# Performance work log

Hardware: AMD Instinct MI355X
Metric: run time of the kernel (lower is better)

Reference implementation:

```python
import jax, jax.numpy as jnp
import numpy as np

N = 100000   # nodes
E = 1600000  # edges (avg degree 16)
G = 64       # graphs in the batch


def setup_inputs() -> dict:
    key = jax.random.key(0)
    ks = jax.random.split(key, 12)
    x = jax.random.normal(ks[0], (N, 1), jnp.float32)
    src = jax.random.randint(ks[1], (E,), 0, N)
    dst = jax.random.randint(ks[2], (E,), 0, N)
    batch = jnp.sort(jax.random.randint(ks[3], (N,), 0, G))
    def glorot(k, shape):
        fan_in, fan_out = shape
        lim = (6.0 / (fan_in + fan_out)) ** 0.5
        return jax.random.uniform(k, shape, jnp.float32, -lim, lim)
    return {
        "x": x, "src": src, "dst": dst, "batch": batch,
        "W1": glorot(ks[4], (1, 100)),   "b1": jnp.zeros((100,), jnp.float32),
        "W2": glorot(ks[5], (100, 200)), "b2": jnp.zeros((200,), jnp.float32),
        "Wl1": glorot(ks[6], (200, 100)), "bl1": jnp.zeros((100,), jnp.float32),
        "Wl2": glorot(ks[7], (100, 1)),   "bl2": jnp.zeros((1,), jnp.float32),
    }


def gcn_layer(x, W, b, src, dst, n_nodes):
    """PyG GCNConv: linear, then sym-normalized aggregation with self-loops, then bias."""
    h = x @ W                                   # [N, out]
    deg = jax.ops.segment_sum(jnp.ones_like(src, dtype=h.dtype), dst,
                              num_segments=n_nodes) + 1.0  # +1 for self-loop
    dinv = jax.lax.rsqrt(deg)                   # [N]
    norm = dinv[src] * dinv[dst]                # [E]
    agg = jax.ops.segment_sum(h[src] * norm[:, None], dst, num_segments=n_nodes)
    agg = agg + h * (dinv * dinv)[:, None]      # self-loop message
    return agg + b


def reference(x, src, dst, batch, W1, b1, W2, b2, Wl1, bl1, Wl2, bl2):
    n = x.shape[0]
    h = jax.nn.silu(gcn_layer(x, W1, b1, src, dst, n))       # [N,100]
    h = jax.nn.silu(gcn_layer(h, W2, b2, src, dst, n))       # [N,200]
    counts = jax.ops.segment_sum(jnp.ones((n,), h.dtype), batch, num_segments=G)
    pooled = jax.ops.segment_sum(h, batch, num_segments=G) / jnp.maximum(counts, 1.0)[:, None]
    h = jax.nn.silu(pooled @ Wl1 + bl1)                      # [G,100]
    out = h @ Wl2 + bl2                                      # [G,1]
    return out.squeeze(-1)                                   # [G]
```

## Files before the change

kernel.cpp:

```cpp
#include <hip/hip_runtime.h>
#include <math.h>

#define F1 100
#define F2 200
#define KM 12
#define BW_LOG 9
#define BW 512

__device__ __forceinline__ float siluf(float v) {
    return v / (1.0f + expf(-v));
}
__device__ __forceinline__ float silu_fast(float v) {
    return __fdividef(v, 1.0f + __expf(-v));
}

#define PREP_BLOCKS 16
__global__ __launch_bounds__(256) void k_prep(
    const int* __restrict__ batch, int N, int G, int nbk,
    int* __restrict__ starts, int* __restrict__ counts,
    double* __restrict__ pooled, int* __restrict__ bcnt, unsigned* __restrict__ amax) {
    int t = threadIdx.x;
    int b = blockIdx.x;
    for (int idx = b * 256 + t; idx < G * F2; idx += PREP_BLOCKS * 256)
        pooled[idx] = 0.0;
    if (b == 1) {
        for (int i = t; i < nbk; i += 256) bcnt[i] = 0;
        if (t == 0) *amax = 0u;
    }
    if (b == 0) {
        if (t <= G) {
            int lo = 0, hi = N;
            while (lo < hi) {
                int mid = (lo + hi) >> 1;
                if (batch[mid] < t) lo = mid + 1; else hi = mid;
            }
            starts[t] = lo;
        }
        __syncthreads();
        if (t < G) counts[t] = starts[t + 1] - starts[t];
    }
}

__global__ __launch_bounds__(256) void k_bucket_count(const int* __restrict__ dst, int E,
                                                      int nbk, int* __restrict__ gcnt) {
    extern __shared__ int cnt[];
    for (int i = threadIdx.x; i < nbk; i += 256) cnt[i] = 0;
    __syncthreads();
    for (int e = blockIdx.x * 256 + threadIdx.x; e < E; e += gridDim.x * 256)
        atomicAdd(&cnt[dst[e] >> BW_LOG], 1);
    __syncthreads();
    for (int i = threadIdx.x; i < nbk; i += 256)
        if (cnt[i]) atomicAdd(&gcnt[i], cnt[i]);
}

__global__ __launch_bounds__(256) void k_bucket_scan(const int* __restrict__ gcnt, int nbk, int E,
                                                     int* __restrict__ base, int* __restrict__ cursor) {
    __shared__ int sh[256];
    int t = threadIdx.x;
    int v = (t < nbk) ? gcnt[t] : 0;
    sh[t] = v;
    __syncthreads();
    for (int ofs = 1; ofs < 256; ofs <<= 1) {
        int u = (t >= ofs) ? sh[t - ofs] : 0;
        __syncthreads();
        sh[t] += u;
        __syncthreads();
    }
    if (t < nbk) { int ex = sh[t] - v; base[t] = ex; cursor[t] = ex; }
    if (t == 0) base[nbk] = E;
}

#define CROUND 4096
#define CEPT 16
__global__ __launch_bounds__(256) void k_bucket_scatter(
    const int* __restrict__ src, const int* __restrict__ dst, int E, int nbk,
    int* __restrict__ gcursor, unsigned long long* __restrict__ pairs) {
    __shared__ int cnt[256];
    __shared__ int scanb[256];
    __shared__ int startx[256];
    __shared__ int cur[256];
    __shared__ int gbase[256];
    __shared__ unsigned long long stage[CROUND];
    int tid = threadIdx.x;
    for (long long r0 = (long long)blockIdx.x * CROUND; r0 < E; r0 += (long long)gridDim.x * CROUND) {
        cnt[tid] = 0;
        __syncthreads();
        int ss[CEPT], dd[CEPT], bb[CEPT];
        bool va[CEPT];
        #pragma unroll
        for (int j = 0; j < CEPT; ++j) {
            long long e = r0 + j * 256 + tid;
            va[j] = (e < E);
            if (va[j]) {
                ss[j] = src[e]; dd[j] = dst[e]; bb[j] = dd[j] >> BW_LOG;
                atomicAdd(&cnt[bb[j]], 1);
            }
        }
        __syncthreads();
        scanb[tid] = cnt[tid];
        __syncthreads();
        for (int ofs = 1; ofs < 256; ofs <<= 1) {
            int u = (tid >= ofs) ? scanb[tid - ofs] : 0;
            __syncthreads();
            scanb[tid] += u;
            __syncthreads();
        }
        int ex = scanb[tid] - cnt[tid];
        startx[tid] = ex;
        cur[tid] = ex;
        if (tid < nbk && cnt[tid] > 0) gbase[tid] = atomicAdd(&gcursor[tid], cnt[tid]);
        __syncthreads();
        int total = scanb[255];
        #pragma unroll
        for (int j = 0; j < CEPT; ++j) {
            if (va[j]) {
                int slot = atomicAdd(&cur[bb[j]], 1);
                stage[slot] = ((unsigned long long)(unsigned)dd[j] << 32) | (unsigned)ss[j];
            }
        }
        __syncthreads();
        for (int i = tid; i < total; i += 256) {
            unsigned long long p = stage[i];
            int b = (int)(p >> 32) >> BW_LOG;
            pairs[gbase[b] + (i - startx[b])] = p;
        }
        __syncthreads();
    }
}

__global__ __launch_bounds__(512) void k_bucket_degoff(
    const unsigned long long* __restrict__ pairs, const int* __restrict__ bbase,
    const float* __restrict__ x, int N,
    float* __restrict__ dinv, float* __restrict__ y, int* __restrict__ off) {
    __shared__ int dl[BW];
    __shared__ int sc[BW];
    int b = blockIdx.x;
    int t = threadIdx.x;
    dl[t] = 0;
    __syncthreads();
    int beg = bbase[b], end = bbase[b + 1];
    for (int i = beg + t; i < end; i += 512)
        atomicAdd(&dl[(int)(pairs[i] >> 32) & (BW - 1)], 1);
    __syncthreads();
    int node = (b << BW_LOG) + t;
    int dg = dl[t];
    if (node < N) {
        float d = 1.0f / sqrtf((float)dg + 1.0f);
        dinv[node] = d;
        y[node] = x[node] * d;
    }
    sc[t] = dg;
    __syncthreads();
    for (int ofs = 1; ofs < BW; ofs <<= 1) {
        int u = (t >= ofs) ? sc[t - ofs] : 0;
        __syncthreads();
        sc[t] += u;
        __syncthreads();
    }
    if (node < N) off[node] = beg + sc[t] - dg;
    if (node == N - 1) off[N] = beg + sc[t];
}

__global__ __launch_bounds__(512) void k_bucket_fill(
    const unsigned long long* __restrict__ pairs, const int* __restrict__ bbase,
    const int* __restrict__ off, const float* __restrict__ y, const float* __restrict__ dinv,
    int N, int* __restrict__ nbr, float2* __restrict__ aggxd, unsigned* __restrict__ amax) {
    __shared__ int offl[BW];
    __shared__ int cur[BW];
    __shared__ float agg[BW];
    int b = blockIdx.x;
    int t = threadIdx.x;
    int node0 = b << BW_LOG;
    int node = node0 + t;
    offl[t] = (node < N) ? off[node] : 0;
    cur[t] = 0;
    agg[t] = 0.0f;
    __syncthreads();
    int beg = bbase[b], end = bbase[b + 1];
    for (int i = beg + t; i < end; i += 512) {
        unsigned long long p = pairs[i];
        int s = (int)(p & 0xffffffffu);
        int d = (int)(p >> 32);
        int l = d & (BW - 1);
        int pos = atomicAdd(&cur[l], 1);
        nbr[offl[l] + pos] = s;
        atomicAdd(&agg[l], y[s]);
    }
    __syncthreads();
    float av = 0.0f;
    if (node < N) {
        float dn = dinv[node];
        float a = dn * (agg[t] + y[node]);
        aggxd[node] = make_float2(a, dn);
        av = fabsf(a);
    }
    __syncthreads();
    agg[t] = av;
    __syncthreads();
    for (int ofs = 256; ofs > 0; ofs >>= 1) {
        if (t < ofs) agg[t] = fmaxf(agg[t], agg[t + ofs]);
        __syncthreads();
    }
    if (t == 0) atomicMax(amax, __float_as_uint(agg[0]));
}

__global__ __launch_bounds__(64) void k_fit_coef(
    const float* __restrict__ W1, const float* __restrict__ b1,
    const unsigned* __restrict__ amax_bits,
    double* __restrict__ cl , float* __restrict__ scal ) {
    int j = blockIdx.x;
    int i = threadIdx.x;
    float A = __uint_as_float(*amax_bits);
    if (!(A > 0.0f)) A = 1.0f;
    A *= 1.000001f;
    if (j == 0 && i == 0) { scal[0] = A; scal[1] = 1.0f / A; }
    const double PI = 3.14159265358979323846;
    double th = (i + 0.5) * (PI / 64.0);
    double xx = cos(th);
    double w = (double)W1[j] * (double)A;
    double u = w * xx + (double)b1[j];
    double f = u / (1.0 + exp(-u));
    double acc[KM];
    {
        double c0 = 1.0, c1 = xx;
        acc[0] = f;
        acc[1] = f * xx;
        #pragma unroll
        for (int k = 2; k < KM; ++k) {
            double c2 = 2.0 * xx * c1 - c0;
            acc[k] = f * c2;
            c0 = c1; c1 = c2;
        }
    }
    #pragma unroll
    for (int k = 0; k < KM; ++k) {
        double v = acc[k];
        for (int ofs = 32; ofs > 0; ofs >>= 1)
            v += __shfl_down(v, ofs);
        if (i == 0) cl[k * F1 + j] = v * ((k == 0 ? 1.0 : 2.0) / 64.0);
    }
}

__global__ __launch_bounds__(256) void k_fit_fold(
    const double* __restrict__ cl, const float* __restrict__ W2,
    float* __restrict__ Dmat ) {
    __shared__ double scl[KM * F1];
    int tid = threadIdx.x;
    for (int idx = tid; idx < KM * F1; idx += 256) scl[idx] = cl[idx];
    __syncthreads();
    int idx = blockIdx.x * 256 + tid;
    if (idx >= KM * F2) return;
    int k = idx / F2, m = idx % F2;
    double s = 0.0;
    #pragma unroll 4
    for (int j = 0; j < F1; ++j)
        s += scl[k * F1 + j] * (double)W2[j * F2 + m];
    Dmat[idx] = (float)s;
}

#define P7_NODES 32
__global__ __launch_bounds__(256) void k_h2_pool7(
    const int* __restrict__ off, const int* __restrict__ nbr,
    const float2* __restrict__ aggxd, const float* __restrict__ scal,
    const float* __restrict__ Dmat, const float* __restrict__ b2,
    const int* __restrict__ batch, int N, double* __restrict__ pooled) {
    __shared__ float sM[P7_NODES][KM];
    __shared__ int sbatch[P7_NODES];
    int tid = threadIdx.x;
    int base = blockIdx.x * P7_NODES;
    if (tid < P7_NODES) {
        int n = base + tid;
        sbatch[tid] = (n < N) ? batch[n] : -1;
    }
    int m = tid;
    bool act = (m < F2);
    float4 d4[KM / 4];
    float bb = 0.0f;
    if (act) {
        #pragma unroll
        for (int k = 0; k < KM / 4; ++k) {
            d4[k].x = Dmat[(4 * k + 0) * F2 + m];
            d4[k].y = Dmat[(4 * k + 1) * F2 + m];
            d4[k].z = Dmat[(4 * k + 2) * F2 + m];
            d4[k].w = Dmat[(4 * k + 3) * F2 + m];
        }
        bb = b2[m];
    }
    {
        int g = tid >> 3;
        int l = tid & 7;
        int node = base + g;
        float invA = scal[1];
        float u[KM];
        #pragma unroll
        for (int k = 0; k < KM; ++k) u[k] = 0.0f;
        if (node < N) {
            int beg = off[node], end = off[node + 1];
            for (int e = beg + l; e < end; e += 8) {
                int s = nbr[e];
                float2 q = aggxd[s];
                float w = q.y;
                float xa = q.x * invA;
                float tx = xa + xa;
                float c0 = 1.0f, c1 = xa;
                u[0] += w;
                u[1] = fmaf(w, c1, u[1]);
                #pragma unroll
                for (int k = 2; k < KM; ++k) {
                    float c2 = fmaf(tx, c1, -c0);
                    u[k] = fmaf(w, c2, u[k]);
                    c0 = c1; c1 = c2;
                }
            }
        }
        #pragma unroll
        for (int k = 0; k < KM; ++k) {
            u[k] += __shfl_down(u[k], 4, 8);
            u[k] += __shfl_down(u[k], 2, 8);
            u[k] += __shfl_down(u[k], 1, 8);
        }
        if (l == 0 && node < N) {
            float2 sd = aggxd[node];
            float d0 = sd.y;
            float d00 = d0 * d0;
            float xa = sd.x * invA;
            float tx = xa + xa;
            float c0 = 1.0f, c1 = xa;
            sM[g][0] = fmaf(d0, u[0], d00);
            sM[g][1] = fmaf(d0, u[1], d00 * xa);
            #pragma unroll
            for (int k = 2; k < KM; ++k) {
                float c2 = fmaf(tx, c1, -c0);
                sM[g][k] = fmaf(d0, u[k], d00 * c2);
                c0 = c1; c1 = c2;
            }
        }
    }
    __syncthreads();
    double pl = 0.0;
    int gcur = -1;
    int nlim = min(P7_NODES, N - base);
    int i = 0;
    for (; i + 1 < nlim; i += 2) {
        float p0 = bb, p1 = 0.f, p2 = 0.f, p3 = 0.f;
        float q0 = bb, q1 = 0.f, q2 = 0.f, q3 = 0.f;
        const float4* mA = (const float4*)&sM[i][0];
        const float4* mB = (const float4*)&sM[i + 1][0];
        #pragma unroll
        for (int k = 0; k < KM / 4; ++k) {
            float4 a = mA[k];
            float4 c = mB[k];
            p0 = fmaf(a.x, d4[k].x, p0); q0 = fmaf(c.x, d4[k].x, q0);
            p1 = fmaf(a.y, d4[k].y, p1); q1 = fmaf(c.y, d4[k].y, q1);
            p2 = fmaf(a.z, d4[k].z, p2); q2 = fmaf(c.z, d4[k].z, q2);
            p3 = fmaf(a.w, d4[k].w, p3); q3 = fmaf(c.w, d4[k].w, q3);
        }
        float preA = (p0 + p1) + (p2 + p3);
        float preB = (q0 + q1) + (q2 + q3);
        float hA = silu_fast(preA);
        float hB = silu_fast(preB);
        int g = sbatch[i];
        if (g != gcur) {
            if (gcur >= 0 && act) atomicAdd(&pooled[(size_t)gcur * F2 + m], pl);
            pl = 0.0;
            gcur = g;
        }
        if (act) pl += (double)hA;
        g = sbatch[i + 1];
        if (g != gcur) {
            if (gcur >= 0 && act) atomicAdd(&pooled[(size_t)gcur * F2 + m], pl);
            pl = 0.0;
            gcur = g;
        }
        if (act) pl += (double)hB;
    }
    if (i < nlim) {
        float p0 = bb, p1 = 0.f, p2 = 0.f, p3 = 0.f;
        const float4* mA = (const float4*)&sM[i][0];
        #pragma unroll
        for (int k = 0; k < KM / 4; ++k) {
            float4 a = mA[k];
            p0 = fmaf(a.x, d4[k].x, p0);
            p1 = fmaf(a.y, d4[k].y, p1);
            p2 = fmaf(a.z, d4[k].z, p2);
            p3 = fmaf(a.w, d4[k].w, p3);
        }
        float pre = (p0 + p1) + (p2 + p3);
        int g = sbatch[i];
        if (g != gcur) {
            if (gcur >= 0 && act) atomicAdd(&pooled[(size_t)gcur * F2 + m], pl);
            pl = 0.0;
            gcur = g;
        }
        if (act) pl += (double)silu_fast(pre);
    }
    if (gcur >= 0 && act) atomicAdd(&pooled[(size_t)gcur * F2 + m], pl);
}

#define SCHUNK 2048
__global__ __launch_bounds__(256) void k_scan_partial(const int* __restrict__ deg, int N,
                                                      int* __restrict__ partials) {
    __shared__ int red[256];
    int base = blockIdx.x * SCHUNK;
    int s = 0;
    for (int i = threadIdx.x; i < SCHUNK; i += 256) {
        int idx = base + i;
        if (idx < N) s += deg[idx];
    }
    red[threadIdx.x] = s;
    __syncthreads();
    for (int ofs = 128; ofs > 0; ofs >>= 1) {
        if (threadIdx.x < ofs) red[threadIdx.x] += red[threadIdx.x + ofs];
        __syncthreads();
    }
    if (threadIdx.x == 0) partials[blockIdx.x] = red[0];
}
__global__ __launch_bounds__(1024) void k_scan_blocks(int* __restrict__ partials, int nb) {
    __shared__ int sh[1024];
    int t = threadIdx.x;
    int v = (t < nb) ? partials[t] : 0;
    sh[t] = v;
    __syncthreads();
    for (int ofs = 1; ofs < 1024; ofs <<= 1) {
        int u = (t >= ofs) ? sh[t - ofs] : 0;
        __syncthreads();
        sh[t] += u;
        __syncthreads();
    }
    if (t < nb) partials[t] = sh[t] - v;
}
__global__ __launch_bounds__(256) void k_scan_final(const int* __restrict__ deg, int N,
                                                    const int* __restrict__ partials,
                                                    int* __restrict__ off) {
    __shared__ int sh[256];
    int base = blockIdx.x * SCHUNK;
    int i0 = base + threadIdx.x * 8;
    int v[8];
    int s = 0;
    #pragma unroll
    for (int j = 0; j < 8; ++j) {
        int idx = i0 + j;
        v[j] = (idx < N) ? deg[idx] : 0;
        s += v[j];
    }
    int mine = s;
    sh[threadIdx.x] = s;
    __syncthreads();
    for (int ofs = 1; ofs < 256; ofs <<= 1) {
        int u = (threadIdx.x >= ofs) ? sh[threadIdx.x - ofs] : 0;
        __syncthreads();
        sh[threadIdx.x] += u;
        __syncthreads();
    }
    int run = partials[blockIdx.x] + sh[threadIdx.x] - mine;
    #pragma unroll
    for (int j = 0; j < 8; ++j) {
        int idx = i0 + j;
        if (idx < N) { off[idx] = run; run += v[j]; }
    }
    if (N >= i0 && N <= i0 + 8) off[N] = run;
}
__global__ void k_count_deg(const int* __restrict__ dst, int E, int* __restrict__ deg) {
    int i = blockIdx.x * blockDim.x + threadIdx.x;
    if (i < E) atomicAdd(&deg[dst[i]], 1);
}
__global__ void k_dinv_self(const int* __restrict__ deg, const float* __restrict__ x, int N,
                            float* __restrict__ dinv, float* __restrict__ aggx) {
    int i = blockIdx.x * blockDim.x + threadIdx.x;
    if (i < N) {
        float d = 1.0f / sqrtf((float)deg[i] + 1.0f);
        dinv[i] = d;
        aggx[i] = x[i] * d * d;
    }
}
__global__ void k_fill_agg(const int* __restrict__ src, const int* __restrict__ dst, int E,
                           const int* __restrict__ off, int* __restrict__ cursor,
                           int* __restrict__ nbr,
                           const float* __restrict__ x, const float* __restrict__ dinv,
                           float* __restrict__ aggx) {
    int e = blockIdx.x * blockDim.x + threadIdx.x;
    if (e < E) {
        int s = src[e], d = dst[e];
        int p = atomicAdd(&cursor[d], 1);
        nbr[off[d] + p] = s;
        atomicAdd(&aggx[d], x[s] * dinv[s] * dinv[d]);
    }
}
__global__ __launch_bounds__(256) void k_aggh(
    const int* __restrict__ off, const int* __restrict__ nbr,
    const float* __restrict__ aggx, const float* __restrict__ dinv,
    const float* __restrict__ W1, const float* __restrict__ b1,
    int N, float* __restrict__ aggh) {
    int wave = threadIdx.x >> 6;
    int lane = threadIdx.x & 63;
    int n = blockIdx.x * 4 + wave;
    if (n >= N) return;
    int ja = lane, jb = lane + 64;
    float w1a = (ja < F1) ? W1[ja] : 0.0f;
    float b1a = (ja < F1) ? b1[ja] : 0.0f;
    float w1b = (jb < F1) ? W1[jb] : 0.0f;
    float b1b = (jb < F1) ? b1[jb] : 0.0f;
    float d0 = dinv[n];
    float a0 = aggx[n];
    float accA = silu_fast(fmaf(a0, w1a, b1a)) * (d0 * d0);
    float accB = silu_fast(fmaf(a0, w1b, b1b)) * (d0 * d0);
    int beg = off[n], end = off[n + 1];
    for (int t = beg; t < end; t += 64) {
        int cnt = min(64, end - t);
        float sa = 0.0f, sw = 0.0f;
        if (lane < cnt) {
            int s = nbr[t + lane];
            sa = aggx[s];
            sw = dinv[s] * d0;
        }
        for (int i = 0; i < cnt; ++i) {
            float ai = __shfl(sa, i);
            float wi = __shfl(sw, i);
            accA = fmaf(wi, silu_fast(fmaf(ai, w1a, b1a)), accA);
            accB = fmaf(wi, silu_fast(fmaf(ai, w1b, b1b)), accB);
        }
    }
    if (ja < F1) aggh[(size_t)n * F1 + ja] = accA;
    if (jb < F1) aggh[(size_t)n * F1 + jb] = accB;
}
#define HP_NODES 20
#define HP_KT 25
__global__ __launch_bounds__(256) void k_h2_pool3(
    const float* __restrict__ aggh, const float* __restrict__ W2, const float* __restrict__ b2,
    const int* __restrict__ batch, int N, double* __restrict__ pooled) {
    __shared__ float smem[HP_KT * F2 + HP_NODES * (F1 + 1)];
    float* sW = smem;
    float* sA = smem + HP_KT * F2;
    float* sOut = smem;
    __shared__ int sbatch[HP_NODES];
    int tid = threadIdx.x;
    int base = blockIdx.x * HP_NODES;
    for (int idx = tid; idx < HP_NODES * (F1 / 4); idx += 256) {
        int i = idx / (F1 / 4), q = idx % (F1 / 4);
        int n = base + i;
        float4 v = make_float4(0.f, 0.f, 0.f, 0.f);
        if (n < N) v = *(const float4*)(aggh + (size_t)n * F1 + q * 4);
        float* dp = &sA[i * (F1 + 1) + q * 4];
        dp[0] = v.x; dp[1] = v.y; dp[2] = v.z; dp[3] = v.w;
    }
    if (tid < HP_NODES) {
        int n = base + tid;
        sbatch[tid] = (n < N) ? batch[n] : -1;
    }
    const int fgrp = tid % 50;
    const int ngrp = tid / 50;
    const int m0 = fgrp * 4;
    const int i0 = ngrp * 4;
    const bool act = (tid < 250);
    float acc[4][4];
    #pragma unroll
    for (int i = 0; i < 4; ++i)
        #pragma unroll
        for (int j = 0; j < 4; ++j) acc[i][j] = 0.0f;
    for (int kt = 0; kt < F1; kt += HP_KT) {
        __syncthreads();
        for (int idx = tid; idx < (HP_KT * F2) / 4; idx += 256)
            ((float4*)sW)[idx] = ((const float4*)(W2 + (size_t)kt * F2))[idx];
        __syncthreads();
        if (act) {
            #pragma unroll
            for (int kk = 0; kk < HP_KT; ++kk) {
                float4 w = *(const float4*)&sW[kk * F2 + m0];
                int k = kt + kk;
                float a0 = sA[(i0 + 0) * (F1 + 1) + k];
                float a1 = sA[(i0 + 1) * (F1 + 1) + k];
                float a2 = sA[(i0 + 2) * (F1 + 1) + k];
                float a3 = sA[(i0 + 3) * (F1 + 1) + k];
                acc[0][0] = fmaf(a0, w.x, acc[0][0]); acc[0][1] = fmaf(a0, w.y, acc[0][1]);
                acc[0][2] = fmaf(a0, w.z, acc[0][2]); acc[0][3] = fmaf(a0, w.w, acc[0][3]);
                acc[1][0] = fmaf(a1, w.x, acc[1][0]); acc[1][1] = fmaf(a1, w.y, acc[1][1]);
                acc[1][2] = fmaf(a1, w.z, acc[1][2]); acc[1][3] = fmaf(a1, w.w, acc[1][3]);
                acc[2][0] = fmaf(a2, w.x, acc[2][0]); acc[2][1] = fmaf(a2, w.y, acc[2][1]);
                acc[2][2] = fmaf(a2, w.z, acc[2][2]); acc[2][3] = fmaf(a2, w.w, acc[2][3]);
                acc[3][0] = fmaf(a3, w.x, acc[3][0]); acc[3][1] = fmaf(a3, w.y, acc[3][1]);
                acc[3][2] = fmaf(a3, w.z, acc[3][2]); acc[3][3] = fmaf(a3, w.w, acc[3][3]);
            }
        }
    }
    __syncthreads();
    if (act) {
        float4 bb = *(const float4*)(b2 + m0);
        #pragma unroll
        for (int i = 0; i < 4; ++i) {
            float4 r;
            r.x = siluf(acc[i][0] + bb.x);
            r.y = siluf(acc[i][1] + bb.y);
            r.z = siluf(acc[i][2] + bb.z);
            r.w = siluf(acc[i][3] + bb.w);
            *(float4*)&sOut[(i0 + i) * F2 + m0] = r;
        }
    }
    __syncthreads();
    if (tid < F2) {
        double pl = 0.0;
        int gcur = -1;
        for (int i = 0; i < HP_NODES; ++i) {
            int n = base + i;
            if (n >= N) break;
            int g = sbatch[i];
            if (g != gcur) {
                if (gcur >= 0) atomicAdd(&pooled[(size_t)gcur * F2 + tid], pl);
                pl = 0.0;
                gcur = g;
            }
            pl += (double)sOut[i * F2 + tid];
        }
        if (gcur >= 0) atomicAdd(&pooled[(size_t)gcur * F2 + tid], pl);
    }
}

__global__ __launch_bounds__(256) void k_head(
    const double* __restrict__ pooled, const int* __restrict__ counts,
    const float* __restrict__ Wl1, const float* __restrict__ bl1,
    const float* __restrict__ Wl2, const float* __restrict__ bl2,
    float* __restrict__ out) {
    int g = blockIdx.x;
    int tid = threadIdx.x;
    __shared__ double sp[F2];
    __shared__ double red[256];
    double icnt = 1.0 / (double)max(counts[g], 1);
    for (int m = tid; m < F2; m += 256) sp[m] = pooled[(size_t)g * F2 + m] * icnt;
    __syncthreads();
    double part = 0.0;
    if (tid < 100) {
        double acc = (double)bl1[tid];
        #pragma unroll 4
        for (int m = 0; m < F2; ++m) acc += sp[m] * (double)Wl1[m * 100 + tid];
        double t1 = acc / (1.0 + exp(-acc));
        part = t1 * (double)Wl2[tid];
    }
    red[tid] = part;
    __syncthreads();
    for (int s = 128; s > 0; s >>= 1) {
        if (tid < s) red[tid] += red[tid + s];
        __syncthreads();
    }
    if (tid == 0) out[g] = (float)(red[0] + (double)bl2[0]);
}

extern "C" void kernel_launch(void* const* d_in, const int* in_sizes, int n_in,
                              void* d_out, int out_size, void* d_ws, size_t ws_size,
                              hipStream_t stream)
{
    const float* x   = (const float*)d_in[0];
    const int*   src = (const int*)d_in[1];
    const int*   dst = (const int*)d_in[2];
    const int*   batch = (const int*)d_in[3];
    const float* W1  = (const float*)d_in[4];
    const float* b1  = (const float*)d_in[5];
    const float* W2  = (const float*)d_in[6];
    const float* b2  = (const float*)d_in[7];
    const float* Wl1 = (const float*)d_in[8];
    const float* bl1 = (const float*)d_in[9];
    const float* Wl2 = (const float*)d_in[10];
    const float* bl2 = (const float*)d_in[11];
    int N = in_sizes[0];
    int E = in_sizes[1];
    int G = out_size;
    float* out = (float*)d_out;

    char* ws = (char*)d_ws;
    size_t o = 0;
    auto alloc = [&](size_t bytes) -> void* {
        o = (o + 255) & ~(size_t)255;
        void* p = ws + o;
        o += bytes;
        return p;
    };
    int nscan = (N + SCHUNK - 1) / SCHUNK;
    int nbk = (N + BW - 1) / BW;
    int*    deg    = (int*)alloc((size_t)N * 4);
    int*    cursor = (int*)alloc((size_t)N * 4);
    int*    off    = (int*)alloc((size_t)(N + 1) * 4);
    int*    nbr    = (int*)alloc((size_t)E * 4);
    float*  dinv   = (float*)alloc((size_t)N * 4);
    float*  aggx   = (float*)alloc((size_t)N * 4);
    float*  yv     = (float*)alloc((size_t)N * 4);
    float*  aggh   = (float*)alloc((size_t)N * F1 * 4);
    double* pooled = (double*)alloc((size_t)G * F2 * 8);
    int*    counts = (int*)alloc((size_t)G * 4);
    int*    starts = (int*)alloc((size_t)(G + 1) * 4);
    int*    partials = (int*)alloc((size_t)nscan * 4);
    int*    bcnt   = (int*)alloc((size_t)nbk * 4);
    int*    bbase  = (int*)alloc((size_t)(nbk + 1) * 4);
    int*    bcur   = (int*)alloc((size_t)nbk * 4);
    float2* aggxd  = (float2*)alloc((size_t)N * 8);
    float*  Dmat   = (float*)alloc((size_t)KM * F2 * 4);
    double* clbuf  = (double*)alloc((size_t)KM * F1 * 8);
    float*  scal   = (float*)alloc(2 * 4);
    unsigned* amaxb = (unsigned*)alloc(4);
    o = (o + 255) & ~(size_t)255;
    unsigned long long* pairs = (unsigned long long*)(ws + o);
    bool use_bucket = (o + (size_t)E * 8) <= ws_size;

    int tE = (E + 255) / 256;
    int tN = (N + 255) / 256;

    if (use_bucket) {
        k_prep<<<PREP_BLOCKS, 256, 0, stream>>>(batch, N, G, nbk, starts, counts, pooled, bcnt, amaxb);
        k_bucket_count<<<240, 256, nbk * 4, stream>>>(dst, E, nbk, bcnt);
        k_bucket_scan<<<1, 256, 0, stream>>>(bcnt, nbk, E, bbase, bcur);
        k_bucket_scatter<<<240, 256, 0, stream>>>(src, dst, E, nbk, bcur, pairs);
        k_bucket_degoff<<<nbk, 512, 0, stream>>>(pairs, bbase, x, N, dinv, yv, off);
        k_bucket_fill<<<nbk, 512, 0, stream>>>(pairs, bbase, off, yv, dinv, N, nbr, aggxd, amaxb);
        k_fit_coef<<<F1, 64, 0, stream>>>(W1, b1, amaxb, clbuf, scal);
        k_fit_fold<<<(KM * F2 + 255) / 256, 256, 0, stream>>>(clbuf, W2, Dmat);
        k_h2_pool7<<<(N + P7_NODES - 1) / P7_NODES, 256, 0, stream>>>(
            off, nbr, aggxd, scal, Dmat, b2, batch, N, pooled);
    } else {
        k_prep<<<PREP_BLOCKS, 256, 0, stream>>>(batch, N, G, nbk, starts, counts, pooled, bcnt, amaxb);
        hipMemsetAsync(deg, 0, (size_t)N * 4, stream);
        hipMemsetAsync(cursor, 0, (size_t)N * 4, stream);
        k_count_deg<<<tE, 256, 0, stream>>>(dst, E, deg);
        k_dinv_self<<<tN, 256, 0, stream>>>(deg, x, N, dinv, aggx);
        k_scan_partial<<<nscan, 256, 0, stream>>>(deg, N, partials);
        k_scan_blocks<<<1, 1024, 0, stream>>>(partials, nscan);
        k_scan_final<<<nscan, 256, 0, stream>>>(deg, N, partials, off);
        k_fill_agg<<<tE, 256, 0, stream>>>(src, dst, E, off, cursor, nbr, x, dinv, aggx);
        k_aggh<<<(N + 3) / 4, 256, 0, stream>>>(off, nbr, aggx, dinv, W1, b1, N, aggh);
        k_h2_pool3<<<(N + HP_NODES - 1) / HP_NODES, 256, 0, stream>>>(aggh, W2, b2, batch, N, pooled);
    }
    k_head<<<G, 256, 0, stream>>>(pooled, counts, Wl1, bl1, Wl2, bl2, out);
}
```

Before: 139.5 us.

## Fuse bucket CSR build kernels into one persistent kernel with grid barriers

Replaces the five separate bucket kernels (count, scan, scatter, degree/offset, fill) with a single persistent 240-block kernel. The stages are separated by atomic-counter grid barriers, and the block size grows from 256 to 512 threads with CEPT halved. The aim is to remove several kernel launch gaps and the tail drain between dependent stages. The trade-off is spin-wait barrier cost, correctness that relies on all 240 blocks being co-resident, and fewer blocks (240 instead of nbk) working on the per-bucket stages.

```diff
diff --git a/kernel.cpp b/kernel.cpp
--- a/kernel.cpp
+++ b/kernel.cpp
@@ -18,7 +18,8 @@
 __global__ __launch_bounds__(256) void k_prep(
     const int* __restrict__ batch, int N, int G, int nbk,
     int* __restrict__ starts, int* __restrict__ counts,
-    double* __restrict__ pooled, int* __restrict__ bcnt, unsigned* __restrict__ amax) {
+    double* __restrict__ pooled, int* __restrict__ bcnt, unsigned* __restrict__ amax,
+    int* __restrict__ gbar) {
     int t = threadIdx.x;
     int b = blockIdx.x;
     for (int idx = b * 256 + t; idx < G * F2; idx += PREP_BLOCKS * 256)
@@ -26,6 +27,7 @@
     if (b == 1) {
         for (int i = t; i < nbk; i += 256) bcnt[i] = 0;
         if (t == 0) *amax = 0u;
+        if (t < 8) gbar[t] = 0;
     }
     if (b == 0) {
         if (t <= G) {
@@ -41,167 +43,186 @@
     }
 }
 
-__global__ __launch_bounds__(256) void k_bucket_count(const int* __restrict__ dst, int E,
-                                                      int nbk, int* __restrict__ gcnt) {
-    extern __shared__ int cnt[];
-    for (int i = threadIdx.x; i < nbk; i += 256) cnt[i] = 0;
-    __syncthreads();
-    for (int e = blockIdx.x * 256 + threadIdx.x; e < E; e += gridDim.x * 256)
-        atomicAdd(&cnt[dst[e] >> BW_LOG], 1);
-    __syncthreads();
-    for (int i = threadIdx.x; i < nbk; i += 256)
-        if (cnt[i]) atomicAdd(&gcnt[i], cnt[i]);
-}
-
-__global__ __launch_bounds__(256) void k_bucket_scan(const int* __restrict__ gcnt, int nbk, int E,
-                                                     int* __restrict__ base, int* __restrict__ cursor) {
-    __shared__ int sh[256];
-    int t = threadIdx.x;
-    int v = (t < nbk) ? gcnt[t] : 0;
-    sh[t] = v;
-    __syncthreads();
-    for (int ofs = 1; ofs < 256; ofs <<= 1) {
-        int u = (t >= ofs) ? sh[t - ofs] : 0;
-        __syncthreads();
-        sh[t] += u;
-        __syncthreads();
-    }
-    if (t < nbk) { int ex = sh[t] - v; base[t] = ex; cursor[t] = ex; }
-    if (t == 0) base[nbk] = E;
-}
-
+__device__ __forceinline__ void gsync(int* ctr, int nblk) {
+    __syncthreads();
+    if (threadIdx.x == 0) {
+        __threadfence();
+        atomicAdd(ctr, 1);
+        while (atomicAdd(ctr, 0) < nblk) { }
+        __threadfence();
+    }
+    __syncthreads();
+}
+
+#define GB_BLOCKS 240
 #define CROUND 4096
-#define CEPT 16
-__global__ __launch_bounds__(256) void k_bucket_scatter(
-    const int* __restrict__ src, const int* __restrict__ dst, int E, int nbk,
-    int* __restrict__ gcursor, unsigned long long* __restrict__ pairs) {
-    __shared__ int cnt[256];
-    __shared__ int scanb[256];
-    __shared__ int startx[256];
-    __shared__ int cur[256];
-    __shared__ int gbase[256];
-    __shared__ unsigned long long stage[CROUND];
+#define CEPT 8
+__global__ __launch_bounds__(512) void k_bucket_build(
+    const int* __restrict__ src, const int* __restrict__ dst,
+    const float* __restrict__ x, int N, int E, int nbk,
+    int* __restrict__ bcnt, int* __restrict__ bbase, int* __restrict__ bcur,
+    unsigned long long* __restrict__ pairs,
+    float* __restrict__ dinv, float* __restrict__ y, int* __restrict__ off,
+    int* __restrict__ nbr, float2* __restrict__ aggxd, unsigned* __restrict__ amax,
+    int* __restrict__ gbar) {
+    __shared__ __align__(16) char raw[43008];
     int tid = threadIdx.x;
-    for (long long r0 = (long long)blockIdx.x * CROUND; r0 < E; r0 += (long long)gridDim.x * CROUND) {
-        cnt[tid] = 0;
-        __syncthreads();
-        int ss[CEPT], dd[CEPT], bb[CEPT];
-        bool va[CEPT];
-        #pragma unroll
-        for (int j = 0; j < CEPT; ++j) {
-            long long e = r0 + j * 256 + tid;
-            va[j] = (e < E);
-            if (va[j]) {
-                ss[j] = src[e]; dd[j] = dst[e]; bb[j] = dd[j] >> BW_LOG;
-                atomicAdd(&cnt[bb[j]], 1);
-            }
-        }
-        __syncthreads();
-        scanb[tid] = cnt[tid];
-        __syncthreads();
-        for (int ofs = 1; ofs < 256; ofs <<= 1) {
-            int u = (tid >= ofs) ? scanb[tid - ofs] : 0;
-            __syncthreads();
-            scanb[tid] += u;
-            __syncthreads();
-        }
-        int ex = scanb[tid] - cnt[tid];
-        startx[tid] = ex;
-        cur[tid] = ex;
-        if (tid < nbk && cnt[tid] > 0) gbase[tid] = atomicAdd(&gcursor[tid], cnt[tid]);
-        __syncthreads();
-        int total = scanb[255];
-        #pragma unroll
-        for (int j = 0; j < CEPT; ++j) {
-            if (va[j]) {
-                int slot = atomicAdd(&cur[bb[j]], 1);
-                stage[slot] = ((unsigned long long)(unsigned)dd[j] << 32) | (unsigned)ss[j];
-            }
-        }
-        __syncthreads();
-        for (int i = tid; i < total; i += 256) {
-            unsigned long long p = stage[i];
-            int b = (int)(p >> 32) >> BW_LOG;
-            pairs[gbase[b] + (i - startx[b])] = p;
-        }
-        __syncthreads();
-    }
-}
-
-__global__ __launch_bounds__(512) void k_bucket_degoff(
-    const unsigned long long* __restrict__ pairs, const int* __restrict__ bbase,
-    const float* __restrict__ x, int N,
-    float* __restrict__ dinv, float* __restrict__ y, int* __restrict__ off) {
-    __shared__ int dl[BW];
-    __shared__ int sc[BW];
-    int b = blockIdx.x;
-    int t = threadIdx.x;
-    dl[t] = 0;
-    __syncthreads();
-    int beg = bbase[b], end = bbase[b + 1];
-    for (int i = beg + t; i < end; i += 512)
-        atomicAdd(&dl[(int)(pairs[i] >> 32) & (BW - 1)], 1);
-    __syncthreads();
-    int node = (b << BW_LOG) + t;
-    int dg = dl[t];
-    if (node < N) {
-        float d = 1.0f / sqrtf((float)dg + 1.0f);
-        dinv[node] = d;
-        y[node] = x[node] * d;
-    }
-    sc[t] = dg;
-    __syncthreads();
-    for (int ofs = 1; ofs < BW; ofs <<= 1) {
-        int u = (t >= ofs) ? sc[t - ofs] : 0;
-        __syncthreads();
-        sc[t] += u;
-        __syncthreads();
-    }
-    if (node < N) off[node] = beg + sc[t] - dg;
-    if (node == N - 1) off[N] = beg + sc[t];
-}
-
-__global__ __launch_bounds__(512) void k_bucket_fill(
-    const unsigned long long* __restrict__ pairs, const int* __restrict__ bbase,
-    const int* __restrict__ off, const float* __restrict__ y, const float* __restrict__ dinv,
-    int N, int* __restrict__ nbr, float2* __restrict__ aggxd, unsigned* __restrict__ amax) {
-    __shared__ int offl[BW];
-    __shared__ int cur[BW];
-    __shared__ float agg[BW];
-    int b = blockIdx.x;
-    int t = threadIdx.x;
-    int node0 = b << BW_LOG;
-    int node = node0 + t;
-    offl[t] = (node < N) ? off[node] : 0;
-    cur[t] = 0;
-    agg[t] = 0.0f;
-    __syncthreads();
-    int beg = bbase[b], end = bbase[b + 1];
-    for (int i = beg + t; i < end; i += 512) {
-        unsigned long long p = pairs[i];
-        int s = (int)(p & 0xffffffffu);
-        int d = (int)(p >> 32);
-        int l = d & (BW - 1);
-        int pos = atomicAdd(&cur[l], 1);
-        nbr[offl[l] + pos] = s;
-        atomicAdd(&agg[l], y[s]);
-    }
-    __syncthreads();
-    float av = 0.0f;
-    if (node < N) {
-        float dn = dinv[node];
-        float a = dn * (agg[t] + y[node]);
-        aggxd[node] = make_float2(a, dn);
-        av = fabsf(a);
-    }
-    __syncthreads();
-    agg[t] = av;
-    __syncthreads();
-    for (int ofs = 256; ofs > 0; ofs >>= 1) {
-        if (t < ofs) agg[t] = fmaxf(agg[t], agg[t + ofs]);
-        __syncthreads();
-    }
-    if (t == 0) atomicMax(amax, __float_as_uint(agg[0]));
+    int bid = blockIdx.x;
+
+    {
+        int* hist = (int*)raw;
+        for (int i = tid; i < nbk; i += 512) hist[i] = 0;
+        __syncthreads();
+        for (int e = bid * 512 + tid; e < E; e += GB_BLOCKS * 512)
+            atomicAdd(&hist[dst[e] >> BW_LOG], 1);
+        __syncthreads();
+        for (int i = tid; i < nbk; i += 512)
+            if (hist[i]) atomicAdd(&bcnt[i], hist[i]);
+    }
+    gsync(&gbar[0], GB_BLOCKS);
+
+    if (bid == 0) {
+        int* sh = (int*)raw;
+        int v = (tid < nbk) ? bcnt[tid] : 0;
+        sh[tid] = v;
+        __syncthreads();
+        for (int ofs = 1; ofs < 512; ofs <<= 1) {
+            int u = (tid >= ofs) ? sh[tid - ofs] : 0;
+            __syncthreads();
+            sh[tid] += u;
+            __syncthreads();
+        }
+        if (tid < nbk) { int ex = sh[tid] - v; bbase[tid] = ex; bcur[tid] = ex; }
+        if (tid == 0) bbase[nbk] = E;
+    }
+    gsync(&gbar[1], GB_BLOCKS);
+
+    {
+        unsigned long long* stage = (unsigned long long*)raw;
+        int* cnt    = (int*)(raw + 32768);
+        int* scanb  = (int*)(raw + 34816);
+        int* startx = (int*)(raw + 36864);
+        int* cur    = (int*)(raw + 38912);
+        int* gbase  = (int*)(raw + 40960);
+        for (long long r0 = (long long)bid * CROUND; r0 < E; r0 += (long long)GB_BLOCKS * CROUND) {
+            cnt[tid] = 0;
+            __syncthreads();
+            int ss[CEPT], dd[CEPT], bb[CEPT];
+            bool va[CEPT];
+            #pragma unroll
+            for (int j = 0; j < CEPT; ++j) {
+                long long e = r0 + j * 512 + tid;
+                va[j] = (e < E);
+                if (va[j]) {
+                    ss[j] = src[e]; dd[j] = dst[e]; bb[j] = dd[j] >> BW_LOG;
+                    atomicAdd(&cnt[bb[j]], 1);
+                }
+            }
+            __syncthreads();
+            scanb[tid] = cnt[tid];
+            __syncthreads();
+            for (int ofs = 1; ofs < 512; ofs <<= 1) {
+                int u = (tid >= ofs) ? scanb[tid - ofs] : 0;
+                __syncthreads();
+                scanb[tid] += u;
+                __syncthreads();
+            }
+            int ex = scanb[tid] - cnt[tid];
+            startx[tid] = ex;
+            cur[tid] = ex;
+            if (tid < nbk && cnt[tid] > 0) gbase[tid] = atomicAdd(&bcur[tid], cnt[tid]);
+            __syncthreads();
+            int total = scanb[511];
+            #pragma unroll
+            for (int j = 0; j < CEPT; ++j) {
+                if (va[j]) {
+                    int slot = atomicAdd(&cur[bb[j]], 1);
+                    stage[slot] = ((unsigned long long)(unsigned)dd[j] << 32) | (unsigned)ss[j];
+                }
+            }
+            __syncthreads();
+            for (int i = tid; i < total; i += 512) {
+                unsigned long long p = stage[i];
+                int b = (int)(p >> 32) >> BW_LOG;
+                pairs[gbase[b] + (i - startx[b])] = p;
+            }
+            __syncthreads();
+        }
+    }
+    gsync(&gbar[2], GB_BLOCKS);
+
+    {
+        int* dl = (int*)raw;
+        int* sc = (int*)(raw + 2048);
+        for (int b = bid; b < nbk; b += GB_BLOCKS) {
+            dl[tid] = 0;
+            __syncthreads();
+            int beg = bbase[b], end = bbase[b + 1];
+            for (int i = beg + tid; i < end; i += 512)
+                atomicAdd(&dl[(int)(pairs[i] >> 32) & (BW - 1)], 1);
+            __syncthreads();
+            int node = (b << BW_LOG) + tid;
+            int dg = dl[tid];
+            if (node < N) {
+                float d = 1.0f / sqrtf((float)dg + 1.0f);
+                dinv[node] = d;
+                y[node] = x[node] * d;
+            }
+            sc[tid] = dg;
+            __syncthreads();
+            for (int ofs = 1; ofs < BW; ofs <<= 1) {
+                int u = (tid >= ofs) ? sc[tid - ofs] : 0;
+                __syncthreads();
+                sc[tid] += u;
+                __syncthreads();
+            }
+            if (node < N) off[node] = beg + sc[tid] - dg;
+            if (node == N - 1) off[N] = beg + sc[tid];
+            __syncthreads();
+        }
+    }
+    gsync(&gbar[3], GB_BLOCKS);
+
+    {
+        int* offl  = (int*)raw;
+        int* cur   = (int*)(raw + 2048);
+        float* agg = (float*)(raw + 4096);
+        for (int b = bid; b < nbk; b += GB_BLOCKS) {
+            int node0 = b << BW_LOG;
+            int node = node0 + tid;
+            offl[tid] = (node < N) ? off[node] : 0;
+            cur[tid] = 0;
+            agg[tid] = 0.0f;
+            __syncthreads();
+            int beg = bbase[b], end = bbase[b + 1];
+            for (int i = beg + tid; i < end; i += 512) {
+                unsigned long long p = pairs[i];
+                int s = (int)(p & 0xffffffffu);
+                int d = (int)(p >> 32);
+                int l = d & (BW - 1);
+                int pos = atomicAdd(&cur[l], 1);
+                nbr[offl[l] + pos] = s;
+                atomicAdd(&agg[l], y[s]);
+            }
+            __syncthreads();
+            float av = 0.0f;
+            if (node < N) {
+                float dn = dinv[node];
+                float a = dn * (agg[tid] + y[node]);
+                aggxd[node] = make_float2(a, dn);
+                av = fabsf(a);
+            }
+            __syncthreads();
+            agg[tid] = av;
+            __syncthreads();
+            for (int ofs = 256; ofs > 0; ofs >>= 1) {
+                if (tid < ofs) agg[tid] = fmaxf(agg[tid], agg[tid + ofs]);
+                __syncthreads();
+            }
+            if (tid == 0) atomicMax(amax, __float_as_uint(agg[0]));
+            __syncthreads();
+        }
+    }
 }
 
 __global__ __launch_bounds__(64) void k_fit_coef(
@@ -694,26 +715,25 @@
     double* clbuf  = (double*)alloc((size_t)KM * F1 * 8);
     float*  scal   = (float*)alloc(2 * 4);
     unsigned* amaxb = (unsigned*)alloc(4);
+    int*    gbar   = (int*)alloc(8 * 4);
     o = (o + 255) & ~(size_t)255;
     unsigned long long* pairs = (unsigned long long*)(ws + o);
-    bool use_bucket = (o + (size_t)E * 8) <= ws_size;
+    bool use_bucket = ((o + (size_t)E * 8) <= ws_size) && (nbk <= 512);
 
     int tE = (E + 255) / 256;
     int tN = (N + 255) / 256;
 
     if (use_bucket) {
-        k_prep<<<PREP_BLOCKS, 256, 0, stream>>>(batch, N, G, nbk, starts, counts, pooled, bcnt, amaxb);
-        k_bucket_count<<<240, 256, nbk * 4, stream>>>(dst, E, nbk, bcnt);
-        k_bucket_scan<<<1, 256, 0, stream>>>(bcnt, nbk, E, bbase, bcur);
-        k_bucket_scatter<<<240, 256, 0, stream>>>(src, dst, E, nbk, bcur, pairs);
-        k_bucket_degoff<<<nbk, 512, 0, stream>>>(pairs, bbase, x, N, dinv, yv, off);
-        k_bucket_fill<<<nbk, 512, 0, stream>>>(pairs, bbase, off, yv, dinv, N, nbr, aggxd, amaxb);
+        k_prep<<<PREP_BLOCKS, 256, 0, stream>>>(batch, N, G, nbk, starts, counts, pooled, bcnt, amaxb, gbar);
+        k_bucket_build<<<GB_BLOCKS, 512, 0, stream>>>(
+            src, dst, x, N, E, nbk, bcnt, bbase, bcur, pairs,
+            dinv, yv, off, nbr, aggxd, amaxb, gbar);
         k_fit_coef<<<F1, 64, 0, stream>>>(W1, b1, amaxb, clbuf, scal);
         k_fit_fold<<<(KM * F2 + 255) / 256, 256, 0, stream>>>(clbuf, W2, Dmat);
         k_h2_pool7<<<(N + P7_NODES - 1) / P7_NODES, 256, 0, stream>>>(
             off, nbr, aggxd, scal, Dmat, b2, batch, N, pooled);
     } else {
-        k_prep<<<PREP_BLOCKS, 256, 0, stream>>>(batch, N, G, nbk, starts, counts, pooled, bcnt, amaxb);
+        k_prep<<<PREP_BLOCKS, 256, 0, stream>>>(batch, N, G, nbk, starts, counts, pooled, bcnt, amaxb, gbar);
         hipMemsetAsync(deg, 0, (size_t)N * 4, stream);
         hipMemsetAsync(cursor, 0, (size_t)N * 4, stream);
         k_count_deg<<<tE, 256, 0, stream>>>(dst, E, deg);
```

Result: slower. 191.2 us (+37.0%).
